# Performance work log

Hardware: AMD Instinct MI355X
Metric: run time of the kernel (lower is better)

The kernel has to match this reference:

```python
import jax, jax.numpy as jnp
import numpy as np

R, H, B = 512, 512, 1024
VOCAB = 1000


def setup_inputs() -> dict:
    key = jax.random.key(0)
    k1, k2 = jax.random.split(key)
    ref = jax.random.randint(k1, (R, B), 0, VOCAB)
    hyp = jax.random.randint(k2, (H, B), 0, VOCAB)
    return {"ref": ref, "hyp": hyp}


def reference(ref, hyp):
    """Levenshtein edit distance (eos=None, uniform unit costs, norm=False).

    ref: (R, B) int tokens, hyp: (H, B) int tokens. Returns (B,) float distances.
    Matches torch _string_matching with ins=del=sub=1 (mult=1, mistakes folded).
    """
    Rr, Bb = ref.shape
    idx = jnp.arange(Rr + 1, dtype=jnp.float32)[:, None]  # (R+1, 1)
    row0 = jnp.broadcast_to(idx, (Rr + 1, Bb)) * 1.0      # init row: i * del_cost

    def step(row, hyp_t):
        # hyp_t: (B,) current hypothesis token
        neq = (ref != hyp_t[None, :]).astype(jnp.float32)      # (R, B)
        new = row + 1.0                                        # insertion
        sub = row[:-1] + neq                                   # substitution/copy
        new = jnp.concatenate([new[:1], jnp.minimum(new[1:], sub)], axis=0)
        # deletion closure: new_i = min_{j<=i} (new_j + (i-j)); with del=1 this is
        # cummin(new_j - j) + i, a prefix-min along the ref axis.
        new = jax.lax.cummin(new - idx, axis=0) + idx
        return new, None

    row, _ = jax.lax.scan(step, row0, hyp)
    return row[-1]  # distance at ref_len = R, shape (B,)
```

## Files before the change

kernel.cpp:

```cpp
#include <hip/hip_runtime.h>


#define HLEN 512
#define BATCH 1024
#define FAKE2  0x3FFF3FFFu
#define SENT2  0x03FF03FFu
#define BIASHI 0x04000000u
#define ONE2   0x00010001u
#define NEG22  0xFFFEFFFEu

__device__ __forceinline__ unsigned dpp_shr1(unsigned old, unsigned src) {
  return (unsigned)__builtin_amdgcn_update_dpp((int)old, (int)src, 0x138, 0xF, 0xF, false);
}
__device__ __forceinline__ unsigned algn(unsigned hi, unsigned lo) {
  return __builtin_amdgcn_alignbit(hi, lo, 16);
}
__device__ __forceinline__ unsigned pkmin(unsigned a, unsigned b) {
  unsigned d; asm("v_pk_min_u16 %0, %1, %2" : "=v"(d) : "v"(a), "v"(b)); return d;
}
__device__ __forceinline__ unsigned pkadd(unsigned a, unsigned b) {
  unsigned d; asm("v_pk_add_u16 %0, %1, %2" : "=v"(d) : "v"(a), "v"(b)); return d;
}

#define STEP(A2, A1, AN, Q0, Q1, Q2, Q3, tok)                          \
  {                                                                    \
    unsigned dA1 = dpp_shr1(BIASHI, A1[3]);                            \
    unsigned a1s0 = algn(A1[3], dA1);                                  \
    unsigned dHT = dpp_shr1((tok) << 16, Q3);                          \
    unsigned hn = algn(Q3, dHT);                                       \
    unsigned nq0 = pkmin(rt[0] ^ hn, one2);                            \
    unsigned c0  = pkadd(s0c, pkadd(nq0, neg2));                       \
    AN[0] = pkmin(pkmin(a1s0, A1[0]), c0);                             \
    unsigned nq1 = pkmin(rt[1] ^ Q0, one2);                            \
    unsigned c1  = pkadd(A2[0], pkadd(nq1, neg2));                     \
    AN[1] = pkmin(pkmin(A1[0], A1[1]), c1);                            \
    unsigned nq2 = pkmin(rt[2] ^ Q1, one2);                            \
    unsigned c2  = pkadd(A2[1], pkadd(nq2, neg2));                     \
    AN[2] = pkmin(pkmin(A1[1], A1[2]), c2);                            \
    unsigned nq3 = pkmin(rt[3] ^ Q2, one2);                            \
    unsigned c3  = pkadd(A2[2], pkadd(nq3, neg2));                     \
    AN[3] = pkmin(pkmin(A1[2], A1[3]), c3);                            \
    s0c = a1s0;                                                        \
    Q3 = hn;                                                           \
  }

__global__ void __launch_bounds__(64)
edit_distance_kernel(const int* __restrict__ ref,
                     const int* __restrict__ hyp,
                     float* __restrict__ out) {
  const int b = blockIdx.x;
  const int lane = threadIdx.x;

  __shared__ unsigned hyp_s[HLEN];
#pragma unroll
  for (int c = 0; c < HLEN / 64; ++c)
    hyp_s[c * 64 + lane] = (unsigned)hyp[(c * 64 + lane) * BATCH + b];

  unsigned rt[4];
#pragma unroll
  for (int p = 0; p < 4; ++p) {
    unsigned lo = (unsigned)ref[(lane * 8 + p) * BATCH + b];
    unsigned hi = (unsigned)ref[(lane * 8 + p + 4) * BATCH + b];
    rt[p] = lo | (hi << 16);
  }

  __syncthreads();

  const unsigned one2 = ONE2;
  const unsigned neg2 = NEG22;

  unsigned A[4], Bv[4], Cv[4];
#pragma unroll
  for (int p = 0; p < 4; ++p) { A[p] = FAKE2; Bv[p] = FAKE2; }
  if (lane == 0) Bv[0] = 0x3FFF0400u;

  unsigned q0 = SENT2, q1 = SENT2, q2 = SENT2, q3 = SENT2;

  unsigned s0c;
  { unsigned dA0 = dpp_shr1(BIASHI, A[3]); s0c = algn(A[3], dA0); }

  unsigned t[12], tn[12];
#pragma unroll
  for (int j = 0; j < 12; ++j) t[j] = hyp_s[j];

  for (int it = 0; it < 85; ++it) {
    const int base = 12 + it * 12;
#pragma unroll
    for (int j = 0; j < 12; ++j) tn[j] = hyp_s[min(base + j, HLEN - 1)];
    STEP(A, Bv, Cv, q0, q1, q2, q3, t[0]);
    STEP(Bv, Cv, A, q3, q0, q1, q2, t[1]);
    STEP(Cv, A, Bv, q2, q3, q0, q1, t[2]);
    STEP(A, Bv, Cv, q1, q2, q3, q0, t[3]);
    STEP(Bv, Cv, A, q0, q1, q2, q3, t[4]);
    STEP(Cv, A, Bv, q3, q0, q1, q2, t[5]);
    STEP(A, Bv, Cv, q2, q3, q0, q1, t[6]);
    STEP(Bv, Cv, A, q1, q2, q3, q0, t[7]);
    STEP(Cv, A, Bv, q0, q1, q2, q3, t[8]);
    STEP(A, Bv, Cv, q3, q0, q1, q2, t[9]);
    STEP(Bv, Cv, A, q2, q3, q0, q1, t[10]);
    STEP(Cv, A, Bv, q1, q2, q3, q0, t[11]);
#pragma unroll
    for (int j = 0; j < 12; ++j) t[j] = tn[j];
  }

  STEP(A, Bv, Cv, q0, q1, q2, q3, t[0]);
  STEP(Bv, Cv, A, q3, q0, q1, q2, t[1]);
  STEP(Cv, A, Bv, q2, q3, q0, q1, t[2]);

  if (lane == 63) out[b] = (float)(Bv[3] >> 16);
}

extern "C" void kernel_launch(void* const* d_in, const int* in_sizes, int n_in,
                              void* d_out, int out_size, void* d_ws, size_t ws_size,
                              hipStream_t stream) {
  const int* ref = (const int*)d_in[0];
  const int* hyp = (const int*)d_in[1];
  float* out = (float*)d_out;
  edit_distance_kernel<<<BATCH, 64, 0, stream>>>(ref, hyp, out);
}
```

Measured before the change: 130.8 us.

## Split anti-diagonal DP across two waves per batch column with LDS handoff

Splits the 512-long ref axis across two wavefronts per block, each holding 256 rows (2 packed registers per lane instead of 4). Wave 0 runs ahead by one 12-step chunk and passes its boundary values to wave 1 through a double-buffered LDS array, with hyp tokens padded in LDS to skew the second wave. This halves the per-step instruction count on each wave's critical path and doubles the waves available. In exchange it adds a block barrier every 12 steps and a one-chunk pipeline skew.

Measured after the change: 147.0 us. 12.3% more time.

```diff
diff --git a/kernel.cpp b/kernel.cpp
--- a/kernel.cpp
+++ b/kernel.cpp
@@ -4,6 +4,7 @@
 #define HLEN 512
 #define BATCH 1024
 #define FAKE2  0x3FFF3FFFu
+#define SENT   0x000003FFu
 #define SENT2  0x03FF03FFu
 #define BIASHI 0x04000000u
 #define ONE2   0x00010001u
@@ -22,92 +23,126 @@
   unsigned d; asm("v_pk_add_u16 %0, %1, %2" : "=v"(d) : "v"(a), "v"(b)); return d;
 }
 
-#define STEP(A2, A1, AN, Q0, Q1, Q2, Q3, tok)                          \
-  {                                                                    \
-    unsigned dA1 = dpp_shr1(BIASHI, A1[3]);                            \
-    unsigned a1s0 = algn(A1[3], dA1);                                  \
-    unsigned dHT = dpp_shr1((tok) << 16, Q3);                          \
-    unsigned hn = algn(Q3, dHT);                                       \
-    unsigned nq0 = pkmin(rt[0] ^ hn, one2);                            \
-    unsigned c0  = pkadd(s0c, pkadd(nq0, neg2));                       \
-    AN[0] = pkmin(pkmin(a1s0, A1[0]), c0);                             \
-    unsigned nq1 = pkmin(rt[1] ^ Q0, one2);                            \
-    unsigned c1  = pkadd(A2[0], pkadd(nq1, neg2));                     \
-    AN[1] = pkmin(pkmin(A1[0], A1[1]), c1);                            \
-    unsigned nq2 = pkmin(rt[2] ^ Q1, one2);                            \
-    unsigned c2  = pkadd(A2[1], pkadd(nq2, neg2));                     \
-    AN[2] = pkmin(pkmin(A1[1], A1[2]), c2);                            \
-    unsigned nq3 = pkmin(rt[3] ^ Q2, one2);                            \
-    unsigned c3  = pkadd(A2[2], pkadd(nq3, neg2));                     \
-    AN[3] = pkmin(pkmin(A1[2], A1[3]), c3);                            \
-    s0c = a1s0;                                                        \
-    Q3 = hn;                                                           \
+#define STEP(A2, A1, AN, QP0, QP1, OLDV, TOK)                        \
+  {                                                                  \
+    unsigned dA1 = dpp_shr1((OLDV), A1[1]);                          \
+    unsigned a1s0 = algn(A1[1], dA1);                                \
+    unsigned dHT = dpp_shr1((TOK) << 16, QP1);                       \
+    unsigned hn = algn(QP1, dHT);                                    \
+    unsigned nq0 = pkmin(rt0 ^ hn, one2);                            \
+    unsigned c0  = pkadd(s0c, pkadd(nq0, neg2));                     \
+    AN[0] = pkmin(pkmin(a1s0, A1[0]), c0);                           \
+    unsigned nq1 = pkmin(rt1 ^ QP0, one2);                           \
+    unsigned c1  = pkadd(A2[0], pkadd(nq1, neg2));                   \
+    AN[1] = pkmin(pkmin(A1[0], A1[1]), c1);                          \
+    s0c = a1s0;                                                      \
+    QP1 = hn;                                                        \
   }
 
-__global__ void __launch_bounds__(64)
+__global__ void __launch_bounds__(128)
 edit_distance_kernel(const int* __restrict__ ref,
                      const int* __restrict__ hyp,
                      float* __restrict__ out) {
   const int b = blockIdx.x;
-  const int lane = threadIdx.x;
+  const int tid = threadIdx.x;
+  const int lane = tid & 63;
+  const int wave = tid >> 6;
 
-  __shared__ unsigned hyp_s[HLEN];
-#pragma unroll
-  for (int c = 0; c < HLEN / 64; ++c)
-    hyp_s[c * 64 + lane] = (unsigned)hyp[(c * 64 + lane) * BATCH + b];
+  __shared__ unsigned hs[1332];
+  __shared__ unsigned buf[2][12];
 
-  unsigned rt[4];
-#pragma unroll
-  for (int p = 0; p < 4; ++p) {
-    unsigned lo = (unsigned)ref[(lane * 8 + p) * BATCH + b];
-    unsigned hi = (unsigned)ref[(lane * 8 + p + 4) * BATCH + b];
-    rt[p] = lo | (hi << 16);
+  for (int i = tid; i < 288; i += 128) hs[i] = SENT;
+  for (int i = tid; i < 512; i += 128) hs[288 + i] = (unsigned)hyp[i * BATCH + b];
+  {
+    unsigned last = (unsigned)hyp[511 * BATCH + b];
+    for (int i = 800 + tid; i < 1332; i += 128) hs[i] = last;
+  }
+  if (tid < 24) ((unsigned*)buf)[tid] = FAKE2;
+
+  const int C = wave << 8;
+  unsigned rt0, rt1;
+  {
+    unsigned e0 = (unsigned)ref[(C + 4 * lane + 0) * BATCH + b];
+    unsigned e2 = (unsigned)ref[(C + 4 * lane + 2) * BATCH + b];
+    unsigned e1 = (unsigned)ref[(C + 4 * lane + 1) * BATCH + b];
+    unsigned e3 = (unsigned)ref[(C + 4 * lane + 3) * BATCH + b];
+    rt0 = e0 | (e2 << 16);
+    rt1 = e1 | (e3 << 16);
+  }
+  __syncthreads();
+
+  const unsigned one2 = ONE2, neg2 = NEG22;
+  unsigned A[2], Bv[2], Cv[2];
+  A[0] = A[1] = Bv[0] = Bv[1] = FAKE2;
+  unsigned q0 = SENT2, q1 = SENT2;
+  unsigned s0c = FAKE2;
+  unsigned scarry = FAKE2;
+  if (wave == 0 && lane == 0) {
+    Bv[0] = 0x3FFF0400u;
+    s0c   = 0x3FFF0400u;
   }
 
-  __syncthreads();
-
-  const unsigned one2 = ONE2;
-  const unsigned neg2 = NEG22;
-
-  unsigned A[4], Bv[4], Cv[4];
-#pragma unroll
-  for (int p = 0; p < 4; ++p) { A[p] = FAKE2; Bv[p] = FAKE2; }
-  if (lane == 0) Bv[0] = 0x3FFF0400u;
-
-  unsigned q0 = SENT2, q1 = SENT2, q2 = SENT2, q3 = SENT2;
-
-  unsigned s0c;
-  { unsigned dA0 = dpp_shr1(BIASHI, A[3]); s0c = algn(A[3], dA0); }
-
-  unsigned t[12], tn[12];
-#pragma unroll
-  for (int j = 0; j < 12; ++j) t[j] = hyp_s[j];
-
-  for (int it = 0; it < 85; ++it) {
-    const int base = 12 + it * 12;
-#pragma unroll
-    for (int j = 0; j < 12; ++j) tn[j] = hyp_s[min(base + j, HLEN - 1)];
-    STEP(A, Bv, Cv, q0, q1, q2, q3, t[0]);
-    STEP(Bv, Cv, A, q3, q0, q1, q2, t[1]);
-    STEP(Cv, A, Bv, q2, q3, q0, q1, t[2]);
-    STEP(A, Bv, Cv, q1, q2, q3, q0, t[3]);
-    STEP(Bv, Cv, A, q0, q1, q2, q3, t[4]);
-    STEP(Cv, A, Bv, q3, q0, q1, q2, t[5]);
-    STEP(A, Bv, Cv, q2, q3, q0, q1, t[6]);
-    STEP(Bv, Cv, A, q1, q2, q3, q0, t[7]);
-    STEP(Cv, A, Bv, q0, q1, q2, q3, t[8]);
-    STEP(A, Bv, Cv, q3, q0, q1, q2, t[9]);
-    STEP(Bv, Cv, A, q2, q3, q0, q1, t[10]);
-    STEP(Cv, A, Bv, q1, q2, q3, q0, t[11]);
-#pragma unroll
-    for (int j = 0; j < 12; ++j) t[j] = tn[j];
+  for (int n = 0; n < 86; ++n) {
+    if (wave == 0) {
+      const int tb = 288 + 12 * n;
+      uint4 ta = *((const uint4*)&hs[tb]);
+      uint4 tm = *((const uint4*)&hs[tb + 4]);
+      uint4 tc = *((const uint4*)&hs[tb + 8]);
+      unsigned s0, s1, s2, s3, s4, s5, s6, s7, s8, s9, s10, s11;
+      STEP(A, Bv, Cv, q0, q1, BIASHI, ta.x);  s0  = Cv[1];
+      STEP(Bv, Cv, A, q1, q0, BIASHI, ta.y);  s1  = A[1];
+      STEP(Cv, A, Bv, q0, q1, BIASHI, ta.z);  s2  = Bv[1];
+      STEP(A, Bv, Cv, q1, q0, BIASHI, ta.w);  s3  = Cv[1];
+      STEP(Bv, Cv, A, q0, q1, BIASHI, tm.x);  s4  = A[1];
+      STEP(Cv, A, Bv, q1, q0, BIASHI, tm.y);  s5  = Bv[1];
+      STEP(A, Bv, Cv, q0, q1, BIASHI, tm.z);  s6  = Cv[1];
+      STEP(Bv, Cv, A, q1, q0, BIASHI, tm.w);  s7  = A[1];
+      STEP(Cv, A, Bv, q0, q1, BIASHI, tc.x);  s8  = Bv[1];
+      STEP(A, Bv, Cv, q1, q0, BIASHI, tc.y);  s9  = Cv[1];
+      STEP(Bv, Cv, A, q0, q1, BIASHI, tc.z);  s10 = A[1];
+      STEP(Cv, A, Bv, q1, q0, BIASHI, tc.w);  s11 = Bv[1];
+      if (lane == 63) {
+        uint4* dst = (uint4*)&buf[n & 1][0];
+        dst[0] = make_uint4(s0, s1, s2, s3);
+        dst[1] = make_uint4(s4, s5, s6, s7);
+        dst[2] = make_uint4(s8, s9, s10, s11);
+      }
+    } else {
+      uint4 sa = *((const uint4*)&buf[(n + 1) & 1][0]);
+      uint4 sb = *((const uint4*)&buf[(n + 1) & 1][4]);
+      uint4 sc = *((const uint4*)&buf[(n + 1) & 1][8]);
+      const int tb = 20 + 12 * n;
+      uint4 ta = *((const uint4*)&hs[tb]);
+      uint4 tm = *((const uint4*)&hs[tb + 4]);
+      uint4 tc = *((const uint4*)&hs[tb + 8]);
+      STEP(A, Bv, Cv, q0, q1, scarry, ta.x);
+      STEP(Bv, Cv, A, q1, q0, sa.x,   ta.y);
+      STEP(Cv, A, Bv, q0, q1, sa.y,   ta.z);
+      STEP(A, Bv, Cv, q1, q0, sa.z,   ta.w);
+      STEP(Bv, Cv, A, q0, q1, sa.w,   tm.x);
+      STEP(Cv, A, Bv, q1, q0, sb.x,   tm.y);
+      STEP(A, Bv, Cv, q0, q1, sb.y,   tm.z);
+      STEP(Bv, Cv, A, q1, q0, sb.z,   tm.w);
+      STEP(Cv, A, Bv, q0, q1, sb.w,   tc.x);
+      STEP(A, Bv, Cv, q1, q0, sc.x,   tc.y);
+      STEP(Bv, Cv, A, q0, q1, sc.y,   tc.z);
+      STEP(Cv, A, Bv, q1, q0, sc.z,   tc.w);
+      scarry = sc.w;
+    }
+    __syncthreads();
   }
 
-  STEP(A, Bv, Cv, q0, q1, q2, q3, t[0]);
-  STEP(Bv, Cv, A, q3, q0, q1, q2, t[1]);
-  STEP(Cv, A, Bv, q2, q3, q0, q1, t[2]);
-
-  if (lane == 63) out[b] = (float)(Bv[3] >> 16);
+  if (wave == 1) {
+    unsigned s0 = buf[1][0];
+    unsigned s1 = buf[1][1];
+    unsigned t0 = hs[20 + 12 * 86];
+    unsigned t1 = hs[20 + 12 * 86 + 1];
+    unsigned t2 = hs[20 + 12 * 86 + 2];
+    STEP(A, Bv, Cv, q0, q1, scarry, t0);
+    STEP(Bv, Cv, A, q1, q0, s0,     t1);
+    STEP(Cv, A, Bv, q0, q1, s1,     t2);
+    if (lane == 63) out[b] = (float)(Bv[1] >> 16);
+  }
 }
 
 extern "C" void kernel_launch(void* const* d_in, const int* in_sizes, int n_in,
@@ -116,5 +151,5 @@
   const int* ref = (const int*)d_in[0];
   const int* hyp = (const int*)d_in[1];
   float* out = (float*)d_out;
-  edit_distance_kernel<<<BATCH, 64, 0, stream>>>(ref, hyp, out);
+  edit_distance_kernel<<<BATCH, 128, 0, stream>>>(ref, hyp, out);
 }
```

## Split anti-diagonal wavefront into two interleaved half-chains with seam handoff

Applied to the files above, without the earlier changes.

Splits the 512 reference rows into a lower half handled left-to-right (shr DPP) and an upper half handled in reversed lane order (shl DPP), each lane holding 2 packed registers per half instead of 4. The two chains are interleaved step by step, with the lower chain's boundary values passed to the upper chain through a register delay line (seam). The goal is to shorten the per-step dependency chain and give the scheduler two independent chains to overlap, using one wave. Hyp tokens are staged in LDS pre-shifted and padded with sentinels and read as uint4 vectors. The cost is more total steps, since the upper chain starts about 24 steps later, plus extra seam registers.

Result: slower. 134.0 us (+2.4%).

```diff
diff --git a/kernel.cpp b/kernel.cpp
--- a/kernel.cpp
+++ b/kernel.cpp
@@ -5,12 +5,16 @@
 #define BATCH 1024
 #define FAKE2  0x3FFF3FFFu
 #define SENT2  0x03FF03FFu
+#define SENTHI 0x03FF0000u
 #define BIASHI 0x04000000u
 #define ONE2   0x00010001u
 #define NEG22  0xFFFEFFFEu
 
 __device__ __forceinline__ unsigned dpp_shr1(unsigned old, unsigned src) {
   return (unsigned)__builtin_amdgcn_update_dpp((int)old, (int)src, 0x138, 0xF, 0xF, false);
+}
+__device__ __forceinline__ unsigned dpp_shl1(unsigned old, unsigned src) {
+  return (unsigned)__builtin_amdgcn_update_dpp((int)old, (int)src, 0x130, 0xF, 0xF, false);
 }
 __device__ __forceinline__ unsigned algn(unsigned hi, unsigned lo) {
   return __builtin_amdgcn_alignbit(hi, lo, 16);
@@ -22,26 +26,36 @@
   unsigned d; asm("v_pk_add_u16 %0, %1, %2" : "=v"(d) : "v"(a), "v"(b)); return d;
 }
 
-#define STEP(A2, A1, AN, Q0, Q1, Q2, Q3, tok)                          \
-  {                                                                    \
-    unsigned dA1 = dpp_shr1(BIASHI, A1[3]);                            \
-    unsigned a1s0 = algn(A1[3], dA1);                                  \
-    unsigned dHT = dpp_shr1((tok) << 16, Q3);                          \
-    unsigned hn = algn(Q3, dHT);                                       \
-    unsigned nq0 = pkmin(rt[0] ^ hn, one2);                            \
-    unsigned c0  = pkadd(s0c, pkadd(nq0, neg2));                       \
-    AN[0] = pkmin(pkmin(a1s0, A1[0]), c0);                             \
-    unsigned nq1 = pkmin(rt[1] ^ Q0, one2);                            \
-    unsigned c1  = pkadd(A2[0], pkadd(nq1, neg2));                     \
-    AN[1] = pkmin(pkmin(A1[0], A1[1]), c1);                            \
-    unsigned nq2 = pkmin(rt[2] ^ Q1, one2);                            \
-    unsigned c2  = pkadd(A2[1], pkadd(nq2, neg2));                     \
-    AN[2] = pkmin(pkmin(A1[1], A1[2]), c2);                            \
-    unsigned nq3 = pkmin(rt[3] ^ Q2, one2);                            \
-    unsigned c3  = pkadd(A2[2], pkadd(nq3, neg2));                     \
-    AN[3] = pkmin(pkmin(A1[2], A1[3]), c3);                            \
-    s0c = a1s0;                                                        \
-    Q3 = hn;                                                           \
+#define STEP_L(A2, A1, AN, QP0, QP1, TOKD)                          \
+  {                                                                 \
+    unsigned dA1 = dpp_shr1(BIASHI, A1[1]);                         \
+    unsigned a1s0 = algn(A1[1], dA1);                               \
+    unsigned dHT = dpp_shr1((TOKD), QP1);                           \
+    unsigned hn = algn(QP1, dHT);                                   \
+    unsigned nq0 = pkmin(rl0 ^ hn, one2);                           \
+    unsigned c0  = pkadd(s0cl, pkadd(nq0, neg2));                   \
+    AN[0] = pkmin(pkmin(a1s0, A1[0]), c0);                          \
+    unsigned nq1 = pkmin(rl1 ^ QP0, one2);                          \
+    unsigned c1  = pkadd(A2[0], pkadd(nq1, neg2));                  \
+    AN[1] = pkmin(pkmin(A1[0], A1[1]), c1);                         \
+    s0cl = a1s0;                                                    \
+    QP1 = hn;                                                       \
+  }
+
+#define STEP_U(A2, A1, AN, QP0, QP1, TOKD, SEAM)                    \
+  {                                                                 \
+    unsigned dA1 = dpp_shl1((SEAM), A1[1]);                         \
+    unsigned a1s0 = algn(A1[1], dA1);                               \
+    unsigned dHT = dpp_shl1((TOKD), QP1);                           \
+    unsigned hn = algn(QP1, dHT);                                   \
+    unsigned nq0 = pkmin(ru0 ^ hn, one2);                           \
+    unsigned c0  = pkadd(s0cu, pkadd(nq0, neg2));                   \
+    AN[0] = pkmin(pkmin(a1s0, A1[0]), c0);                          \
+    unsigned nq1 = pkmin(ru1 ^ QP0, one2);                          \
+    unsigned c1  = pkadd(A2[0], pkadd(nq1, neg2));                  \
+    AN[1] = pkmin(pkmin(A1[0], A1[1]), c1);                         \
+    s0cu = a1s0;                                                    \
+    QP1 = hn;                                                       \
   }
 
 __global__ void __launch_bounds__(64)
@@ -51,63 +65,102 @@
   const int b = blockIdx.x;
   const int lane = threadIdx.x;
 
-  __shared__ unsigned hyp_s[HLEN];
-#pragma unroll
-  for (int c = 0; c < HLEN / 64; ++c)
-    hyp_s[c * 64 + lane] = (unsigned)hyp[(c * 64 + lane) * BATCH + b];
-
-  unsigned rt[4];
-#pragma unroll
-  for (int p = 0; p < 4; ++p) {
-    unsigned lo = (unsigned)ref[(lane * 8 + p) * BATCH + b];
-    unsigned hi = (unsigned)ref[(lane * 8 + p + 4) * BATCH + b];
-    rt[p] = lo | (hi << 16);
+  __shared__ __align__(16) unsigned hs[1344];
+  for (int i = lane; i < 288; i += 64) hs[i] = SENTHI;
+  for (int i = lane; i < 512; i += 64)
+    hs[288 + i] = ((unsigned)hyp[i * BATCH + b]) << 16;
+  {
+    unsigned last = ((unsigned)hyp[511 * BATCH + b]) << 16;
+    for (int i = 800 + lane; i < 1344; i += 64) hs[i] = last;
   }
 
+  unsigned rl0, rl1, ru0, ru1;
+  {
+    unsigned e0 = (unsigned)ref[(4 * lane + 0) * BATCH + b];
+    unsigned e1 = (unsigned)ref[(4 * lane + 1) * BATCH + b];
+    unsigned e2 = (unsigned)ref[(4 * lane + 2) * BATCH + b];
+    unsigned e3 = (unsigned)ref[(4 * lane + 3) * BATCH + b];
+    rl0 = e0 | (e2 << 16);
+    rl1 = e1 | (e3 << 16);
+    int ub = 256 + 4 * (63 - lane);
+    unsigned f0 = (unsigned)ref[(ub + 0) * BATCH + b];
+    unsigned f1 = (unsigned)ref[(ub + 1) * BATCH + b];
+    unsigned f2 = (unsigned)ref[(ub + 2) * BATCH + b];
+    unsigned f3 = (unsigned)ref[(ub + 3) * BATCH + b];
+    ru0 = f0 | (f2 << 16);
+    ru1 = f1 | (f3 << 16);
+  }
   __syncthreads();
 
-  const unsigned one2 = ONE2;
-  const unsigned neg2 = NEG22;
+  const unsigned one2 = ONE2, neg2 = NEG22;
 
-  unsigned A[4], Bv[4], Cv[4];
-#pragma unroll
-  for (int p = 0; p < 4; ++p) { A[p] = FAKE2; Bv[p] = FAKE2; }
-  if (lane == 0) Bv[0] = 0x3FFF0400u;
+  unsigned AL[2], BL[2], CL[2], AU[2], BU[2], CU[2];
+  AL[0] = AL[1] = BL[0] = BL[1] = FAKE2;
+  AU[0] = AU[1] = BU[0] = BU[1] = FAKE2;
+  unsigned ql0 = SENT2, ql1 = SENT2, qu0 = SENT2, qu1 = SENT2;
+  unsigned s0cl = FAKE2, s0cu = FAKE2;
+  if (lane == 0) { BL[0] = 0x3FFF0400u; s0cl = 0x3FFF0400u; }
 
-  unsigned q0 = SENT2, q1 = SENT2, q2 = SENT2, q3 = SENT2;
+  unsigned sp0 = FAKE2, sp1 = FAKE2, sp2 = FAKE2, sp3 = FAKE2;
+  unsigned sp4 = FAKE2, sp5 = FAKE2, sp6 = FAKE2, sp7 = FAKE2;
+  unsigned sp8 = FAKE2, sp9 = FAKE2, sp10 = FAKE2, sp11 = FAKE2;
+  unsigned scarry = FAKE2;
 
-  unsigned s0c;
-  { unsigned dA0 = dpp_shr1(BIASHI, A[3]); s0c = algn(A[3], dA0); }
+  uint4 tla = *(const uint4*)&hs[288];
+  uint4 tlb = *(const uint4*)&hs[292];
+  uint4 tlc = *(const uint4*)&hs[296];
+  uint4 tua = *(const uint4*)&hs[20];
+  uint4 tub = *(const uint4*)&hs[24];
+  uint4 tuc = *(const uint4*)&hs[28];
 
-  unsigned t[12], tn[12];
-#pragma unroll
-  for (int j = 0; j < 12; ++j) t[j] = hyp_s[j];
+  for (int n = 0; n < 86; ++n) {
+    const int lb = 288 + 12 * (n + 1);
+    const int ub2 = 20 + 12 * (n + 1);
+    uint4 nla = *(const uint4*)&hs[lb];
+    uint4 nlb = *(const uint4*)&hs[lb + 4];
+    uint4 nlc = *(const uint4*)&hs[lb + 8];
+    uint4 nua = *(const uint4*)&hs[ub2];
+    uint4 nub = *(const uint4*)&hs[ub2 + 4];
+    uint4 nuc = *(const uint4*)&hs[ub2 + 8];
+    unsigned sn0, sn1, sn2, sn3, sn4, sn5, sn6, sn7, sn8, sn9, sn10, sn11;
 
-  for (int it = 0; it < 85; ++it) {
-    const int base = 12 + it * 12;
-#pragma unroll
-    for (int j = 0; j < 12; ++j) tn[j] = hyp_s[min(base + j, HLEN - 1)];
-    STEP(A, Bv, Cv, q0, q1, q2, q3, t[0]);
-    STEP(Bv, Cv, A, q3, q0, q1, q2, t[1]);
-    STEP(Cv, A, Bv, q2, q3, q0, q1, t[2]);
-    STEP(A, Bv, Cv, q1, q2, q3, q0, t[3]);
-    STEP(Bv, Cv, A, q0, q1, q2, q3, t[4]);
-    STEP(Cv, A, Bv, q3, q0, q1, q2, t[5]);
-    STEP(A, Bv, Cv, q2, q3, q0, q1, t[6]);
-    STEP(Bv, Cv, A, q1, q2, q3, q0, t[7]);
-    STEP(Cv, A, Bv, q0, q1, q2, q3, t[8]);
-    STEP(A, Bv, Cv, q3, q0, q1, q2, t[9]);
-    STEP(Bv, Cv, A, q2, q3, q0, q1, t[10]);
-    STEP(Cv, A, Bv, q1, q2, q3, q0, t[11]);
-#pragma unroll
-    for (int j = 0; j < 12; ++j) t[j] = tn[j];
+    STEP_L(AL, BL, CL, ql0, ql1, tla.x); sn0 = CL[1];
+    STEP_U(AU, BU, CU, qu0, qu1, tua.x, scarry);
+    STEP_L(BL, CL, AL, ql1, ql0, tla.y); sn1 = AL[1];
+    STEP_U(BU, CU, AU, qu1, qu0, tua.y, sp0);
+    STEP_L(CL, AL, BL, ql0, ql1, tla.z); sn2 = BL[1];
+    STEP_U(CU, AU, BU, qu0, qu1, tua.z, sp1);
+    STEP_L(AL, BL, CL, ql1, ql0, tla.w); sn3 = CL[1];
+    STEP_U(AU, BU, CU, qu1, qu0, tua.w, sp2);
+    STEP_L(BL, CL, AL, ql0, ql1, tlb.x); sn4 = AL[1];
+    STEP_U(BU, CU, AU, qu0, qu1, tub.x, sp3);
+    STEP_L(CL, AL, BL, ql1, ql0, tlb.y); sn5 = BL[1];
+    STEP_U(CU, AU, BU, qu1, qu0, tub.y, sp4);
+    STEP_L(AL, BL, CL, ql0, ql1, tlb.z); sn6 = CL[1];
+    STEP_U(AU, BU, CU, qu0, qu1, tub.z, sp5);
+    STEP_L(BL, CL, AL, ql1, ql0, tlb.w); sn7 = AL[1];
+    STEP_U(BU, CU, AU, qu1, qu0, tub.w, sp6);
+    STEP_L(CL, AL, BL, ql0, ql1, tlc.x); sn8 = BL[1];
+    STEP_U(CU, AU, BU, qu0, qu1, tuc.x, sp7);
+    STEP_L(AL, BL, CL, ql1, ql0, tlc.y); sn9 = CL[1];
+    STEP_U(AU, BU, CU, qu1, qu0, tuc.y, sp8);
+    STEP_L(BL, CL, AL, ql0, ql1, tlc.z); sn10 = AL[1];
+    STEP_U(BU, CU, AU, qu0, qu1, tuc.z, sp9);
+    STEP_L(CL, AL, BL, ql1, ql0, tlc.w); sn11 = BL[1];
+    STEP_U(CU, AU, BU, qu1, qu0, tuc.w, sp10);
+
+    scarry = sp11;
+    sp0 = sn0; sp1 = sn1; sp2 = sn2; sp3 = sn3; sp4 = sn4; sp5 = sn5;
+    sp6 = sn6; sp7 = sn7; sp8 = sn8; sp9 = sn9; sp10 = sn10; sp11 = sn11;
+    tla = nla; tlb = nlb; tlc = nlc;
+    tua = nua; tub = nub; tuc = nuc;
   }
 
-  STEP(A, Bv, Cv, q0, q1, q2, q3, t[0]);
-  STEP(Bv, Cv, A, q3, q0, q1, q2, t[1]);
-  STEP(Cv, A, Bv, q2, q3, q0, q1, t[2]);
+  STEP_U(AU, BU, CU, qu0, qu1, tua.x, scarry);
+  STEP_U(BU, CU, AU, qu1, qu0, tua.y, sp0);
+  STEP_U(CU, AU, BU, qu0, qu1, tua.z, sp1);
 
-  if (lane == 63) out[b] = (float)(Bv[3] >> 16);
+  if (lane == 0) out[b] = (float)(BU[1] >> 16);
 }
 
 extern "C" void kernel_launch(void* const* d_in, const int* in_sizes, int n_in,
```
